# Performance work log

Hardware: AMD Instinct MI355X
Metric: run time of the kernel (lower is better)

## Reference

```python
import jax, jax.numpy as jnp
import numpy as np

W_PAD = 1  # reflection pad / stencil half-width
CLAMP_MIN = 0.071
EPS = 1e-05


def _laplacian_kernel():
    k = 2 * W_PAD + 1
    ker = -jnp.ones((1, 1, k, k, k), dtype=jnp.float32)
    ker = ker.at[0, 0, W_PAD, W_PAD, W_PAD].set(float(k * k * k - 1))
    return ker  # [O=1, I=1, 3, 3, 3]


def _boundary_weight(pred):
    # pred: [B, L, D, H, W] raw logits
    B, L, D, H, Wd = pred.shape
    ps = jax.nn.softmax(pred, axis=1).astype(jnp.float32)
    # reflect-pad spatial dims by 1, then clamp (matches torch: pad then clamp)
    p = jnp.pad(ps, ((0, 0), (0, 0), (1, 1), (1, 1), (1, 1)), mode='reflect')
    p = jnp.clip(p, CLAMP_MIN)
    # single-channel 3x3x3 stencil applied independently per (batch, label)
    x = p.reshape(B * L, 1, D + 2, H + 2, Wd + 2)
    bt = jax.lax.conv_general_dilated(
        x, _laplacian_kernel(), window_strides=(1, 1, 1), padding='VALID',
        dimension_numbers=('NCDHW', 'OIDHW', 'NCDHW'))
    bt = jnp.abs(bt).reshape(B, L, D, H, Wd)
    bt = jax.lax.stop_gradient(bt)  # torch .detach()
    return 0.5 / (bt + 0.5)


def _dice_bpm(y_pred, y_true, bpm):
    vol_axes = tuple(range(2, y_pred.ndim))  # spatial dims
    top = 2.0 * jnp.sum(y_true * y_pred * bpm, axis=vol_axes)
    bottom = jnp.clip(jnp.sum((y_true + y_pred) * bpm, axis=vol_axes), EPS)
    return -jnp.mean(top / bottom)


def setup_inputs() -> dict:
    key = jax.random.key(0)
    k1, k2 = jax.random.split(key)
    shape = (2, 8, 128, 128, 128)
    pred = jax.random.normal(k1, shape, dtype=jnp.float32)
    target = jax.random.uniform(k2, shape, dtype=jnp.float32)
    return {"pred": pred, "target": target}


def reference(pred, target):
    focal_weight = _boundary_weight(pred)
    return _dice_bpm(pred, target, focal_weight)
```

## Files before the change

kernel.cpp:

```cpp
#include <hip/hip_runtime.h>

constexpr int Dd = 128, Hh = 128, Ww = 128;
constexpr int B_ = 2, L_ = 8;
constexpr int HW = Hh * Ww;
constexpr int S_SP = Dd * HW;
constexpr float CLAMP_MIN = 0.071f;
constexpr float EPS = 1e-5f;

constexpr int DCH = 8;
constexpr int NDC = Dd / DCH;
constexpr int HT = 4;
constexpr int NHG = Hh / HT;
constexpr int NBLK = B_ * NDC * NHG;

__global__ __launch_bounds__(256, 2) void fused_kernel(
    const float* __restrict__ pred, const float* __restrict__ tgt,
    float* __restrict__ partial) {
  const int blk = blockIdx.x;
  const int dc = blk & (NDC - 1);
  const int hg = (blk >> 4) & (NHG - 1);
  const int b  = blk >> 9;
  const int tid = threadIdx.x;
  const int wl = tid & 63;
  const int hl = tid >> 6;
  const int h = hg * HT + hl;
  const int w0 = wl * 2;
  const int d0 = dc * DCH;
  const int hm = (h == 0) ? 1 : h - 1;
  const int hp = (h == Hh - 1) ? Hh - 2 : h + 1;
  const float* Pb = pred + (size_t)b * L_ * S_SP;
  const float* Tb = tgt  + (size_t)b * L_ * S_SP;
  const float* rowp[3] = {Pb + (size_t)hm * Ww + w0,
                          Pb + (size_t)h  * Ww + w0,
                          Pb + (size_t)hp * Ww + w0};

  float s2c[L_][2], ps2[L_][2], cprev[L_][2], rawprev[L_][2];
  float top[L_], bot[L_];
#pragma unroll
  for (int l = 0; l < L_; ++l) {
    top[l] = 0.f; bot[l] = 0.f;
    s2c[l][0] = s2c[l][1] = 0.f;
    ps2[l][0] = ps2[l][1] = 0.f;
    cprev[l][0] = cprev[l][1] = 0.f;
    rawprev[l][0] = rawprev[l][1] = 0.f;
  }

  for (int k = 0; k < DCH + 2; ++k) {
    const int t = d0 - 1 + k;
    const int rt = (t < 0) ? 1 : ((t > Dd - 1) ? Dd - 2 : t);
    const size_t poff = (size_t)rt * HW;
    float s2n[L_][2], ctr[L_][2], rawc[L_][2];
#pragma unroll
    for (int l = 0; l < L_; ++l) s2n[l][0] = s2n[l][1] = 0.f;

#pragma unroll
    for (int ri = 0; ri < 3; ++ri) {
      const float* rp = rowp[ri] + poff;
      float2 v[L_];
#pragma unroll
      for (int l = 0; l < L_; ++l)
        v[l] = *(const float2*)(rp + (size_t)l * S_SP);
      float m0 = v[0].x, m1 = v[0].y;
#pragma unroll
      for (int l = 1; l < L_; ++l) { m0 = fmaxf(m0, v[l].x); m1 = fmaxf(m1, v[l].y); }
      float p0[L_], p1[L_];
      float s0 = 0.f, s1 = 0.f;
#pragma unroll
      for (int l = 0; l < L_; ++l) {
        p0[l] = __expf(v[l].x - m0); s0 += p0[l];
        p1[l] = __expf(v[l].y - m1); s1 += p1[l];
      }
      const float i0 = 1.f / s0, i1 = 1.f / s1;
#pragma unroll
      for (int l = 0; l < L_; ++l) {
        p0[l] = fmaxf(p0[l] * i0, CLAMP_MIN);
        p1[l] = fmaxf(p1[l] * i1, CLAMP_MIN);
      }
#pragma unroll
      for (int l = 0; l < L_; ++l) {
        float lf = __shfl_up(p1[l], 1, 64);
        if (wl == 0) lf = p1[l];
        float rf = __shfl_down(p0[l], 1, 64);
        if (wl == 63) rf = p0[l];
        s2n[l][0] += lf + p0[l] + p1[l];
        s2n[l][1] += p0[l] + p1[l] + rf;
        if (ri == 1) {
          ctr[l][0] = p0[l]; ctr[l][1] = p1[l];
          rawc[l][0] = v[l].x; rawc[l][1] = v[l].y;
        }
      }
    }

    if (k >= 2) {
      const int d = t - 1;
      const size_t base = (size_t)d * HW + (size_t)h * Ww + w0;
#pragma unroll
      for (int l = 0; l < L_; ++l) {
        const float2 tv = *(const float2*)(Tb + (size_t)l * S_SP + base);
        {
          float bt = fabsf(27.f * cprev[l][0] - (ps2[l][0] + s2n[l][0]));
          float bw = 0.5f / (bt + 0.5f);
          top[l] += tv.x * rawprev[l][0] * bw;
          bot[l] += (tv.x + rawprev[l][0]) * bw;
        }
        {
          float bt = fabsf(27.f * cprev[l][1] - (ps2[l][1] + s2n[l][1]));
          float bw = 0.5f / (bt + 0.5f);
          top[l] += tv.y * rawprev[l][1] * bw;
          bot[l] += (tv.y + rawprev[l][1]) * bw;
        }
      }
    }

#pragma unroll
    for (int l = 0; l < L_; ++l) {
      ps2[l][0] = s2c[l][0] + s2n[l][0]; ps2[l][1] = s2c[l][1] + s2n[l][1];
      s2c[l][0] = s2n[l][0];             s2c[l][1] = s2n[l][1];
      cprev[l][0] = ctr[l][0];           cprev[l][1] = ctr[l][1];
      rawprev[l][0] = rawc[l][0];        rawprev[l][1] = rawc[l][1];
    }
  }

#pragma unroll
  for (int l = 0; l < L_; ++l) {
#pragma unroll
    for (int o = 32; o > 0; o >>= 1) {
      top[l] += __shfl_down(top[l], o, 64);
      bot[l] += __shfl_down(bot[l], o, 64);
    }
  }
  __shared__ float red[4][16];
  const int wv = tid >> 6;
  if (wl == 0) {
#pragma unroll
    for (int l = 0; l < L_; ++l) {
      red[wv][2 * l]     = top[l];
      red[wv][2 * l + 1] = bot[l];
    }
  }
  __syncthreads();
  if (tid < 16) {
    float s = red[0][tid] + red[1][tid] + red[2][tid] + red[3][tid];
    partial[blk * 16 + tid] = s;
  }
}

__global__ void finalize_kernel(const float* __restrict__ partial, float* __restrict__ out) {
  __shared__ float rr[16];
  const int t = threadIdx.x;
  const int p = t >> 4;
  const int k = t & 15;
  const int b = p >> 3;
  const int l = p & 7;
  float top = 0.f, bot = 0.f;
  for (int m = 0; m < 32; ++m) {
    int blk = b * (NDC * NHG) + k * 32 + m;
    top += partial[blk * 16 + 2 * l];
    bot += partial[blk * 16 + 2 * l + 1];
  }
#pragma unroll
  for (int o = 8; o > 0; o >>= 1) {
    top += __shfl_down(top, o, 16);
    bot += __shfl_down(bot, o, 16);
  }
  if (k == 0) rr[p] = 2.f * top / fmaxf(bot, EPS);
  __syncthreads();
  if (t == 0) {
    float s = 0.f;
#pragma unroll
    for (int i = 0; i < 16; ++i) s += rr[i];
    out[0] = -s / 16.f;
  }
}

extern "C" void kernel_launch(void* const* d_in, const int* in_sizes, int n_in,
                              void* d_out, int out_size, void* d_ws, size_t ws_size,
                              hipStream_t stream) {
  const float* pred = (const float*)d_in[0];
  const float* tgt  = (const float*)d_in[1];
  float* partial = (float*)d_ws;
  fused_kernel<<<NBLK, 256, 0, stream>>>(pred, tgt, partial);
  finalize_kernel<<<1, 256, 0, stream>>>(partial, (float*)d_out);
}
```

Before: 312.1 us.

## Share H-neighbor rows through LDS halo tile with fp16 storage

Each block now loads each (depth, row) slice once, with 6 row slots covering 4 output rows plus a halo, instead of every thread reloading three rows. Horizontal 3-sums and raw logits are kept in shared memory as fp16, and the center softmax is recomputed from the stored raw value and the saved inverse sum. The softmax max-subtraction is dropped. The aim is to cut redundant global loads of pred, roughly 3x, at the cost of two barriers per depth step, idle halo threads in the second phase, and reduced precision from fp16 rounding and the missing max-subtraction.

```diff
diff --git a/kernel.cpp b/kernel.cpp
--- a/kernel.cpp
+++ b/kernel.cpp
@@ -1,4 +1,5 @@
 #include <hip/hip_runtime.h>
+#include <hip/hip_fp16.h>
 
 constexpr int Dd = 128, Hh = 128, Ww = 128;
 constexpr int B_ = 2, L_ = 8;
@@ -13,112 +14,117 @@
 constexpr int NHG = Hh / HT;
 constexpr int NBLK = B_ * NDC * NHG;
 
-__global__ __launch_bounds__(256, 2) void fused_kernel(
+__global__ __launch_bounds__(192, 3) void fused_kernel(
     const float* __restrict__ pred, const float* __restrict__ tgt,
     float* __restrict__ partial) {
   const int blk = blockIdx.x;
-  const int dc = blk & (NDC - 1);
-  const int hg = (blk >> 4) & (NHG - 1);
+  const int hg = blk & 31;
+  const int dc = (blk >> 5) & 15;
   const int b  = blk >> 9;
   const int tid = threadIdx.x;
-  const int wl = tid & 63;
-  const int hl = tid >> 6;
-  const int h = hg * HT + hl;
-  const int w0 = wl * 2;
+  const int slot = tid >> 5;
+  const int wseg = tid & 31;
+  const int w0 = wseg * 4;
+  int r = hg * HT - 1 + slot;
+  r = (r < 0) ? 1 : ((r > Hh - 1) ? Hh - 2 : r);
   const int d0 = dc * DCH;
-  const int hm = (h == 0) ? 1 : h - 1;
-  const int hp = (h == Hh - 1) ? Hh - 2 : h + 1;
+  const bool interior = (slot >= 1 && slot <= 4);
+  const int rowout = hg * HT + slot - 1;
   const float* Pb = pred + (size_t)b * L_ * S_SP;
   const float* Tb = tgt  + (size_t)b * L_ * S_SP;
-  const float* rowp[3] = {Pb + (size_t)hm * Ww + w0,
-                          Pb + (size_t)h  * Ww + w0,
-                          Pb + (size_t)hp * Ww + w0};
 
-  float s2c[L_][2], ps2[L_][2], cprev[L_][2], rawprev[L_][2];
+  __shared__ __half rawh[2][6][L_][Ww];
+  __shared__ __half h3h[6][L_][Ww];
+  __shared__ float red[3][16];
+
+  float ps2[L_][4], s2c[L_][4];
+  float invprev[4];
   float top[L_], bot[L_];
 #pragma unroll
   for (int l = 0; l < L_; ++l) {
     top[l] = 0.f; bot[l] = 0.f;
-    s2c[l][0] = s2c[l][1] = 0.f;
-    ps2[l][0] = ps2[l][1] = 0.f;
-    cprev[l][0] = cprev[l][1] = 0.f;
-    rawprev[l][0] = rawprev[l][1] = 0.f;
+#pragma unroll
+    for (int i = 0; i < 4; ++i) { ps2[l][i] = 0.f; s2c[l][i] = 0.f; }
   }
+  invprev[0] = invprev[1] = invprev[2] = invprev[3] = 0.f;
 
   for (int k = 0; k < DCH + 2; ++k) {
     const int t = d0 - 1 + k;
     const int rt = (t < 0) ? 1 : ((t > Dd - 1) ? Dd - 2 : t);
-    const size_t poff = (size_t)rt * HW;
-    float s2n[L_][2], ctr[L_][2], rawc[L_][2];
+
+    float4 v[L_];
+    const float* pp = Pb + (size_t)rt * HW + r * Ww + w0;
 #pragma unroll
-    for (int l = 0; l < L_; ++l) s2n[l][0] = s2n[l][1] = 0.f;
+    for (int l = 0; l < L_; ++l) v[l] = *(const float4*)(pp + (size_t)l * S_SP);
+#pragma unroll
+    for (int l = 0; l < L_; ++l) {
+      *(__half2*)&rawh[k & 1][slot][l][w0]     = __floats2half2_rn(v[l].x, v[l].y);
+      *(__half2*)&rawh[k & 1][slot][l][w0 + 2] = __floats2half2_rn(v[l].z, v[l].w);
+    }
+    float s0 = 0.f, s1 = 0.f, s2 = 0.f, s3 = 0.f;
+#pragma unroll
+    for (int l = 0; l < L_; ++l) {
+      v[l].x = __expf(v[l].x); s0 += v[l].x;
+      v[l].y = __expf(v[l].y); s1 += v[l].y;
+      v[l].z = __expf(v[l].z); s2 += v[l].z;
+      v[l].w = __expf(v[l].w); s3 += v[l].w;
+    }
+    const float i0 = 1.f / s0, i1 = 1.f / s1, i2 = 1.f / s2, i3 = 1.f / s3;
+#pragma unroll
+    for (int l = 0; l < L_; ++l) {
+      float p0 = fmaxf(v[l].x * i0, CLAMP_MIN);
+      float p1 = fmaxf(v[l].y * i1, CLAMP_MIN);
+      float p2 = fmaxf(v[l].z * i2, CLAMP_MIN);
+      float p3 = fmaxf(v[l].w * i3, CLAMP_MIN);
+      float lf = __shfl_up(p3, 1, 64);
+      if (wseg == 0) lf = p1;
+      float rf = __shfl_down(p0, 1, 64);
+      if (wseg == 31) rf = p2;
+      *(__half2*)&h3h[slot][l][w0]     = __floats2half2_rn(lf + p0 + p1, p0 + p1 + p2);
+      *(__half2*)&h3h[slot][l][w0 + 2] = __floats2half2_rn(p1 + p2 + p3, p2 + p3 + rf);
+    }
+    __syncthreads();
 
+    if (interior) {
+      float4 tv[L_];
+      if (k >= 2) {
+        const float* tp = Tb + (size_t)(t - 1) * HW + rowout * Ww + w0;
 #pragma unroll
-    for (int ri = 0; ri < 3; ++ri) {
-      const float* rp = rowp[ri] + poff;
-      float2 v[L_];
-#pragma unroll
-      for (int l = 0; l < L_; ++l)
-        v[l] = *(const float2*)(rp + (size_t)l * S_SP);
-      float m0 = v[0].x, m1 = v[0].y;
-#pragma unroll
-      for (int l = 1; l < L_; ++l) { m0 = fmaxf(m0, v[l].x); m1 = fmaxf(m1, v[l].y); }
-      float p0[L_], p1[L_];
-      float s0 = 0.f, s1 = 0.f;
-#pragma unroll
-      for (int l = 0; l < L_; ++l) {
-        p0[l] = __expf(v[l].x - m0); s0 += p0[l];
-        p1[l] = __expf(v[l].y - m1); s1 += p1[l];
-      }
-      const float i0 = 1.f / s0, i1 = 1.f / s1;
-#pragma unroll
-      for (int l = 0; l < L_; ++l) {
-        p0[l] = fmaxf(p0[l] * i0, CLAMP_MIN);
-        p1[l] = fmaxf(p1[l] * i1, CLAMP_MIN);
+        for (int l = 0; l < L_; ++l) tv[l] = *(const float4*)(tp + (size_t)l * S_SP);
       }
 #pragma unroll
       for (int l = 0; l < L_; ++l) {
-        float lf = __shfl_up(p1[l], 1, 64);
-        if (wl == 0) lf = p1[l];
-        float rf = __shfl_down(p0[l], 1, 64);
-        if (wl == 63) rf = p0[l];
-        s2n[l][0] += lf + p0[l] + p1[l];
-        s2n[l][1] += p0[l] + p1[l] + rf;
-        if (ri == 1) {
-          ctr[l][0] = p0[l]; ctr[l][1] = p1[l];
-          rawc[l][0] = v[l].x; rawc[l][1] = v[l].y;
+        const float2 u0 = __half22float2(*(const __half2*)&h3h[slot - 1][l][w0]);
+        const float2 u1 = __half22float2(*(const __half2*)&h3h[slot - 1][l][w0 + 2]);
+        const float2 m0 = __half22float2(*(const __half2*)&h3h[slot    ][l][w0]);
+        const float2 m1 = __half22float2(*(const __half2*)&h3h[slot    ][l][w0 + 2]);
+        const float2 d0_ = __half22float2(*(const __half2*)&h3h[slot + 1][l][w0]);
+        const float2 d1_ = __half22float2(*(const __half2*)&h3h[slot + 1][l][w0 + 2]);
+        float s2n[4] = {u0.x + m0.x + d0_.x, u0.y + m0.y + d0_.y,
+                        u1.x + m1.x + d1_.x, u1.y + m1.y + d1_.y};
+        if (k >= 2) {
+          const float2 ra = __half22float2(*(const __half2*)&rawh[(k & 1) ^ 1][slot][l][w0]);
+          const float2 rb = __half22float2(*(const __half2*)&rawh[(k & 1) ^ 1][slot][l][w0 + 2]);
+          const float rw[4] = {ra.x, ra.y, rb.x, rb.y};
+          const float tw[4] = {tv[l].x, tv[l].y, tv[l].z, tv[l].w};
+#pragma unroll
+          for (int i = 0; i < 4; ++i) {
+            float c = fmaxf(__expf(rw[i]) * invprev[i], CLAMP_MIN);
+            float bt = fabsf(27.f * c - (ps2[l][i] + s2n[i]));
+            float bw = 0.5f / (bt + 0.5f);
+            top[l] += tw[i] * rw[i] * bw;
+            bot[l] += (tw[i] + rw[i]) * bw;
+          }
+        }
+#pragma unroll
+        for (int i = 0; i < 4; ++i) {
+          ps2[l][i] = s2c[l][i] + s2n[i];
+          s2c[l][i] = s2n[i];
         }
       }
     }
-
-    if (k >= 2) {
-      const int d = t - 1;
-      const size_t base = (size_t)d * HW + (size_t)h * Ww + w0;
-#pragma unroll
-      for (int l = 0; l < L_; ++l) {
-        const float2 tv = *(const float2*)(Tb + (size_t)l * S_SP + base);
-        {
-          float bt = fabsf(27.f * cprev[l][0] - (ps2[l][0] + s2n[l][0]));
-          float bw = 0.5f / (bt + 0.5f);
-          top[l] += tv.x * rawprev[l][0] * bw;
-          bot[l] += (tv.x + rawprev[l][0]) * bw;
-        }
-        {
-          float bt = fabsf(27.f * cprev[l][1] - (ps2[l][1] + s2n[l][1]));
-          float bw = 0.5f / (bt + 0.5f);
-          top[l] += tv.y * rawprev[l][1] * bw;
-          bot[l] += (tv.y + rawprev[l][1]) * bw;
-        }
-      }
-    }
-
-#pragma unroll
-    for (int l = 0; l < L_; ++l) {
-      ps2[l][0] = s2c[l][0] + s2n[l][0]; ps2[l][1] = s2c[l][1] + s2n[l][1];
-      s2c[l][0] = s2n[l][0];             s2c[l][1] = s2n[l][1];
-      cprev[l][0] = ctr[l][0];           cprev[l][1] = ctr[l][1];
-      rawprev[l][0] = rawc[l][0];        rawprev[l][1] = rawc[l][1];
-    }
+    invprev[0] = i0; invprev[1] = i1; invprev[2] = i2; invprev[3] = i3;
+    __syncthreads();
   }
 
 #pragma unroll
@@ -129,9 +135,8 @@
       bot[l] += __shfl_down(bot[l], o, 64);
     }
   }
-  __shared__ float red[4][16];
   const int wv = tid >> 6;
-  if (wl == 0) {
+  if ((tid & 63) == 0) {
 #pragma unroll
     for (int l = 0; l < L_; ++l) {
       red[wv][2 * l]     = top[l];
@@ -139,10 +144,7 @@
     }
   }
   __syncthreads();
-  if (tid < 16) {
-    float s = red[0][tid] + red[1][tid] + red[2][tid] + red[3][tid];
-    partial[blk * 16 + tid] = s;
-  }
+  if (tid < 16) partial[blk * 16 + tid] = red[0][tid] + red[1][tid] + red[2][tid];
 }
 
 __global__ void finalize_kernel(const float* __restrict__ partial, float* __restrict__ out) {
@@ -154,7 +156,7 @@
   const int l = p & 7;
   float top = 0.f, bot = 0.f;
   for (int m = 0; m < 32; ++m) {
-    int blk = b * (NDC * NHG) + k * 32 + m;
+    int blk = b * 512 + k * 32 + m;
     top += partial[blk * 16 + 2 * l];
     bot += partial[blk * 16 + 2 * l + 1];
   }
@@ -179,6 +181,6 @@
   const float* pred = (const float*)d_in[0];
   const float* tgt  = (const float*)d_in[1];
   float* partial = (float*)d_ws;
-  fused_kernel<<<NBLK, 256, 0, stream>>>(pred, tgt, partial);
+  fused_kernel<<<NBLK, 192, 0, stream>>>(pred, tgt, partial);
   finalize_kernel<<<1, 256, 0, stream>>>(partial, (float*)d_out);
 }
```

Result: no change. 307.3 us (-1.5%).

## Stage shared halo rows in LDS with register prefetch and XCD block swizzle

Applied to the files above, without the earlier changes.

Each block now cooperatively loads the HT+2 halo rows of all labels for a depth plane into a double-buffered shared-memory tile, prefetching the next plane into registers while the current one is processed. The four waves then read their three stencil rows from LDS instead of each issuing separate global loads for overlapping rows. Softmax drops the max subtraction and recomputes exp in a second pass rather than holding all probabilities in registers. Block IDs are also swizzled across the eight XCDs and launch bounds relaxed to one block. The trade-off is more exp work per element, an overflow risk for very large logits, and higher LDS use per block.

```diff
diff --git a/kernel.cpp b/kernel.cpp
--- a/kernel.cpp
+++ b/kernel.cpp
@@ -7,117 +7,129 @@
 constexpr float CLAMP_MIN = 0.071f;
 constexpr float EPS = 1e-5f;
 
-constexpr int DCH = 8;
-constexpr int NDC = Dd / DCH;
-constexpr int HT = 4;
-constexpr int NHG = Hh / HT;
+constexpr int DCH = 8, NDC = Dd / DCH;
+constexpr int HT = 4, NHG = Hh / HT;
 constexpr int NBLK = B_ * NDC * NHG;
+constexpr int NROW = HT + 2;
 
-__global__ __launch_bounds__(256, 2) void fused_kernel(
+__global__ __launch_bounds__(256, 1) void fused_kernel(
     const float* __restrict__ pred, const float* __restrict__ tgt,
     float* __restrict__ partial) {
-  const int blk = blockIdx.x;
-  const int dc = blk & (NDC - 1);
-  const int hg = (blk >> 4) & (NHG - 1);
+  const int bid = blockIdx.x;
+  const int blk = (bid & 7) * (NBLK / 8) + (bid >> 3);
+  const int dc = blk & 15;
+  const int hg = (blk >> 4) & 31;
   const int b  = blk >> 9;
   const int tid = threadIdx.x;
   const int wl = tid & 63;
-  const int hl = tid >> 6;
-  const int h = hg * HT + hl;
+  const int wv = tid >> 6;
   const int w0 = wl * 2;
+  const int h0 = hg * HT;
   const int d0 = dc * DCH;
-  const int hm = (h == 0) ? 1 : h - 1;
-  const int hp = (h == Hh - 1) ? Hh - 2 : h + 1;
+  const int gl = tid >> 5;
+  const int gw = (tid & 31) * 4;
   const float* Pb = pred + (size_t)b * L_ * S_SP;
   const float* Tb = tgt  + (size_t)b * L_ * S_SP;
-  const float* rowp[3] = {Pb + (size_t)hm * Ww + w0,
-                          Pb + (size_t)h  * Ww + w0,
-                          Pb + (size_t)hp * Ww + w0};
 
-  float s2c[L_][2], ps2[L_][2], cprev[L_][2], rawprev[L_][2];
+  int rowIdx[NROW];
+#pragma unroll
+  for (int r = 0; r < NROW; ++r) {
+    int rr = h0 - 1 + r;
+    rowIdx[r] = (rr < 0) ? 1 : ((rr > Hh - 1) ? Hh - 2 : rr);
+  }
+
+  __shared__ float buf[2][NROW][L_][Ww];
+  __shared__ float red[4][16];
+
+  float4 st[NROW];
+  auto STAGE = [&](int t) {
+    const int rt = (t < 0) ? 1 : ((t > Dd - 1) ? Dd - 2 : t);
+    const float* P = Pb + (size_t)gl * S_SP + (size_t)rt * HW + gw;
+#pragma unroll
+    for (int r = 0; r < NROW; ++r)
+      st[r] = *(const float4*)(P + rowIdx[r] * Ww);
+  };
+
+  float ps2[L_][2], s2c[L_][2], cprev[L_][2], rawprev[L_][2];
   float top[L_], bot[L_];
 #pragma unroll
   for (int l = 0; l < L_; ++l) {
     top[l] = 0.f; bot[l] = 0.f;
+    ps2[l][0] = ps2[l][1] = 0.f;
     s2c[l][0] = s2c[l][1] = 0.f;
-    ps2[l][0] = ps2[l][1] = 0.f;
     cprev[l][0] = cprev[l][1] = 0.f;
     rawprev[l][0] = rawprev[l][1] = 0.f;
   }
 
+  STAGE(d0 - 1);
+
   for (int k = 0; k < DCH + 2; ++k) {
     const int t = d0 - 1 + k;
-    const int rt = (t < 0) ? 1 : ((t > Dd - 1) ? Dd - 2 : t);
-    const size_t poff = (size_t)rt * HW;
-    float s2n[L_][2], ctr[L_][2], rawc[L_][2];
-#pragma unroll
-    for (int l = 0; l < L_; ++l) s2n[l][0] = s2n[l][1] = 0.f;
+    const int cb = k & 1;
 
 #pragma unroll
-    for (int ri = 0; ri < 3; ++ri) {
-      const float* rp = rowp[ri] + poff;
-      float2 v[L_];
+    for (int r = 0; r < NROW; ++r)
+      *(float4*)&buf[cb][r][gl][gw] = st[r];
+    if (k < DCH + 1) STAGE(t + 1);
+    asm volatile("s_waitcnt lgkmcnt(0)\n\ts_barrier" ::: "memory");
+
+    float2 tv[L_];
+    if (k >= 2) {
+      const float* tp = Tb + (size_t)(t - 1) * HW + (size_t)(h0 + wv) * Ww + w0;
 #pragma unroll
       for (int l = 0; l < L_; ++l)
-        v[l] = *(const float2*)(rp + (size_t)l * S_SP);
-      float m0 = v[0].x, m1 = v[0].y;
+        tv[l] = *(const float2*)(tp + (size_t)l * S_SP);
+    }
+
+    float sden[3][2];
 #pragma unroll
-      for (int l = 1; l < L_; ++l) { m0 = fmaxf(m0, v[l].x); m1 = fmaxf(m1, v[l].y); }
-      float p0[L_], p1[L_];
-      float s0 = 0.f, s1 = 0.f;
+    for (int ri = 0; ri < 3; ++ri) { sden[ri][0] = 0.f; sden[ri][1] = 0.f; }
+#pragma unroll
+    for (int ri = 0; ri < 3; ++ri)
 #pragma unroll
       for (int l = 0; l < L_; ++l) {
-        p0[l] = __expf(v[l].x - m0); s0 += p0[l];
-        p1[l] = __expf(v[l].y - m1); s1 += p1[l];
+        float2 v = *(const float2*)&buf[cb][wv + ri][l][w0];
+        sden[ri][0] += __expf(v.x);
+        sden[ri][1] += __expf(v.y);
       }
-      const float i0 = 1.f / s0, i1 = 1.f / s1;
+    float inv[3][2];
 #pragma unroll
-      for (int l = 0; l < L_; ++l) {
-        p0[l] = fmaxf(p0[l] * i0, CLAMP_MIN);
-        p1[l] = fmaxf(p1[l] * i1, CLAMP_MIN);
-      }
-#pragma unroll
-      for (int l = 0; l < L_; ++l) {
-        float lf = __shfl_up(p1[l], 1, 64);
-        if (wl == 0) lf = p1[l];
-        float rf = __shfl_down(p0[l], 1, 64);
-        if (wl == 63) rf = p0[l];
-        s2n[l][0] += lf + p0[l] + p1[l];
-        s2n[l][1] += p0[l] + p1[l] + rf;
-        if (ri == 1) {
-          ctr[l][0] = p0[l]; ctr[l][1] = p1[l];
-          rawc[l][0] = v[l].x; rawc[l][1] = v[l].y;
-        }
-      }
-    }
-
-    if (k >= 2) {
-      const int d = t - 1;
-      const size_t base = (size_t)d * HW + (size_t)h * Ww + w0;
-#pragma unroll
-      for (int l = 0; l < L_; ++l) {
-        const float2 tv = *(const float2*)(Tb + (size_t)l * S_SP + base);
-        {
-          float bt = fabsf(27.f * cprev[l][0] - (ps2[l][0] + s2n[l][0]));
-          float bw = 0.5f / (bt + 0.5f);
-          top[l] += tv.x * rawprev[l][0] * bw;
-          bot[l] += (tv.x + rawprev[l][0]) * bw;
-        }
-        {
-          float bt = fabsf(27.f * cprev[l][1] - (ps2[l][1] + s2n[l][1]));
-          float bw = 0.5f / (bt + 0.5f);
-          top[l] += tv.y * rawprev[l][1] * bw;
-          bot[l] += (tv.y + rawprev[l][1]) * bw;
-        }
-      }
+    for (int ri = 0; ri < 3; ++ri) {
+      inv[ri][0] = 1.f / sden[ri][0];
+      inv[ri][1] = 1.f / sden[ri][1];
     }
 
 #pragma unroll
     for (int l = 0; l < L_; ++l) {
-      ps2[l][0] = s2c[l][0] + s2n[l][0]; ps2[l][1] = s2c[l][1] + s2n[l][1];
-      s2c[l][0] = s2n[l][0];             s2c[l][1] = s2n[l][1];
-      cprev[l][0] = ctr[l][0];           cprev[l][1] = ctr[l][1];
-      rawprev[l][0] = rawc[l][0];        rawprev[l][1] = rawc[l][1];
+      float s2n0 = 0.f, s2n1 = 0.f;
+      float c0 = 0.f, c1 = 0.f, r0 = 0.f, r1 = 0.f;
+#pragma unroll
+      for (int ri = 0; ri < 3; ++ri) {
+        float2 v = *(const float2*)&buf[cb][wv + ri][l][w0];
+        float p0 = fmaxf(__expf(v.x) * inv[ri][0], CLAMP_MIN);
+        float p1 = fmaxf(__expf(v.y) * inv[ri][1], CLAMP_MIN);
+        float lf = __shfl_up(p1, 1, 64);
+        if (wl == 0) lf = p1;
+        float rf = __shfl_down(p0, 1, 64);
+        if (wl == 63) rf = p0;
+        s2n0 += lf + p0 + p1;
+        s2n1 += p0 + p1 + rf;
+        if (ri == 1) { c0 = p0; c1 = p1; r0 = v.x; r1 = v.y; }
+      }
+      if (k >= 2) {
+        float bt0 = fabsf(27.f * cprev[l][0] - (ps2[l][0] + s2n0));
+        float bw0 = 0.5f / (bt0 + 0.5f);
+        top[l] += tv[l].x * rawprev[l][0] * bw0;
+        bot[l] += (tv[l].x + rawprev[l][0]) * bw0;
+        float bt1 = fabsf(27.f * cprev[l][1] - (ps2[l][1] + s2n1));
+        float bw1 = 0.5f / (bt1 + 0.5f);
+        top[l] += tv[l].y * rawprev[l][1] * bw1;
+        bot[l] += (tv[l].y + rawprev[l][1]) * bw1;
+      }
+      ps2[l][0] = s2c[l][0] + s2n0; ps2[l][1] = s2c[l][1] + s2n1;
+      s2c[l][0] = s2n0;             s2c[l][1] = s2n1;
+      cprev[l][0] = c0;             cprev[l][1] = c1;
+      rawprev[l][0] = r0;           rawprev[l][1] = r1;
     }
   }
 
@@ -129,8 +141,6 @@
       bot[l] += __shfl_down(bot[l], o, 64);
     }
   }
-  __shared__ float red[4][16];
-  const int wv = tid >> 6;
   if (wl == 0) {
 #pragma unroll
     for (int l = 0; l < L_; ++l) {
@@ -154,7 +164,7 @@
   const int l = p & 7;
   float top = 0.f, bot = 0.f;
   for (int m = 0; m < 32; ++m) {
-    int blk = b * (NDC * NHG) + k * 32 + m;
+    int blk = b * 512 + k * 32 + m;
     top += partial[blk * 16 + 2 * l];
     bot += partial[blk * 16 + 2 * l + 1];
   }
```

New measurement: 343.5 us. 10.1% more time.
